# Kernel optimization log

Measured on AMD Instinct MI355X. Metric: run time of the kernel, lower is better.

Reference implementation:

```python
import jax, jax.numpy as jnp
import numpy as np


def setup_inputs() -> dict:
    key = jax.random.key(0)
    kq, kk, kv = jax.random.split(key, 3)
    # transpose_batch_sequence=True layout: [seq, batch, heads, head_dim]
    query = jax.random.normal(kq, (2048, 2, 32, 128), dtype=jnp.float32)
    k = jax.random.normal(kk, (2048, 2, 8, 128), dtype=jnp.float32)
    v = jax.random.normal(kv, (2048, 2, 8, 128), dtype=jnp.float32)
    return {"query": query, "key": k, "value": v}


def reference(query, key, value):
    # scale_attn_logits=True
    head_dim = query.shape[-1]
    q = query / jnp.sqrt(jnp.asarray(head_dim, dtype=query.dtype))
    h_q, h_kv = q.shape[-2], key.shape[-2]
    group_size = h_q // h_kv
    # [q, b, h_kv, g, d]
    gq = q.reshape((*q.shape[:2], h_kv, group_size, q.shape[-1]))
    # scores: [b, h_kv, g, q, k]
    attn = jnp.einsum('qbhgd,kbhd->bhgqk', gq, key)
    attn = jax.nn.softmax(attn, axis=-1)
    # output: [q, b, h_kv, g, d] -> [q, b, h_q, d]
    out = jnp.einsum('bhgqk,kbhd->qbhgd', attn, value)
    return out.reshape(query.shape)
```

## Files before the change

kernel.cpp:

```cpp
#include <hip/hip_runtime.h>

#define SEQ   2048
#define NB    2
#define NHQ   32
#define NHKV  8
#define HD    128
#define QTILE 128
#define QW    32
#define KVB   32
#define NT    (SEQ / KVB)
#define SCALE 0.08838834764831845f
#define QSCALE (0.08838834764831845f * 1.4426950408889634f)
#define THRL2 11.5f

#define QSTRIDE (NB * NHQ * HD)
#define KSTRIDE (NB * NHKV * HD)

typedef float f32x4  __attribute__((ext_vector_type(4)));
typedef float f32x16 __attribute__((ext_vector_type(16)));
typedef __bf16 bf16x8 __attribute__((ext_vector_type(8)));
typedef unsigned short ushort8 __attribute__((ext_vector_type(8)));
typedef unsigned int u32;
typedef unsigned int u32x2 __attribute__((ext_vector_type(2)));
typedef unsigned int u32x4 __attribute__((ext_vector_type(4)));

__device__ __forceinline__ unsigned short f2bf(float f) {
    union { float f; unsigned u; } c; c.f = f;
    return (unsigned short)((c.u + 0x7fffu + ((c.u >> 16) & 1u)) >> 16);
}

__device__ __forceinline__ void gload_lds16(const unsigned short* g, unsigned short* l) {
    __builtin_amdgcn_global_load_lds((const __attribute__((address_space(1))) u32*)g,
                                     (__attribute__((address_space(3))) u32*)l, 16, 0, 0);
}

__device__ __forceinline__ float ex2(float x) {
#if __has_builtin(__builtin_amdgcn_exp2f)
    return __builtin_amdgcn_exp2f(x);
#else
    return exp2f(x);
#endif
}

__device__ __forceinline__ u32 cvtpk(float lo, float hi) {
    u32 r;
    asm("v_cvt_pk_bf16_f32 %0, %1, %2" : "=v"(r) : "v"(lo), "v"(hi));
    return r;
}

__device__ __forceinline__ void pl32swap(u32& a, u32& b) {
#if __has_builtin(__builtin_amdgcn_permlane32_swap)
    u32x2 r = __builtin_amdgcn_permlane32_swap(a, b, false, false);
    a = r.x; b = r.y;
#else
    asm("v_permlane32_swap_b32 %0, %1" : "+v"(a), "+v"(b));
#endif
}

template <int B>
__device__ __forceinline__ bf16x8 make_pa(const f32x16 p) {
    u32 w0 = cvtpk(p[B + 0], p[B + 1]);
    u32 w2 = cvtpk(p[B + 4], p[B + 5]);
    pl32swap(w0, w2);
    u32 w1 = cvtpk(p[B + 2], p[B + 3]);
    u32 w3 = cvtpk(p[B + 6], p[B + 7]);
    pl32swap(w1, w3);
    u32x4 v = {w0, w1, w2, w3};
    return __builtin_bit_cast(bf16x8, v);
}

__global__ __launch_bounds__(256) void conv_k(const float* __restrict__ K,
                                              unsigned short* __restrict__ Kf) {
    __shared__ float tile[32][129];
    int t  = blockIdx.x & 63;
    int bh = blockIdx.x >> 6;
#pragma unroll
    for (int i = 0; i < 4; ++i) {
        int f4 = i * 256 + threadIdx.x;
        int r = f4 >> 5, d4 = (f4 & 31) * 4;
        float4 v = *(const float4*)(K + ((size_t)(t * 32 + r) * 16 + bh) * 128 + d4);
        tile[r][d4] = v.x; tile[r][d4 + 1] = v.y;
        tile[r][d4 + 2] = v.z; tile[r][d4 + 3] = v.w;
    }
    __syncthreads();
#pragma unroll
    for (int i = 0; i < 2; ++i) {
        int lin = i * 256 + threadIdx.x;
        int r = lin & 31, c = lin >> 5;
        ushort8 u;
#pragma unroll
        for (int j = 0; j < 8; ++j) u[j] = f2bf(tile[r][c * 8 + j]);
        *(ushort8*)&Kf[((size_t)(bh * 64 + t) * 16 + c) * 256 + r * 8] = u;
    }
}

__global__ __launch_bounds__(256) void conv_v(const float* __restrict__ V,
                                              unsigned short* __restrict__ Vf) {
    __shared__ float tile[32][129];
    int t  = blockIdx.x & 63;
    int bh = blockIdx.x >> 6;
#pragma unroll
    for (int i = 0; i < 4; ++i) {
        int f4 = i * 256 + threadIdx.x;
        int kv = f4 >> 5, d4 = (f4 & 31) * 4;
        float4 v = *(const float4*)(V + ((size_t)(t * 32 + kv) * 16 + bh) * 128 + d4);
        tile[kv][d4] = v.x; tile[kv][d4 + 1] = v.y;
        tile[kv][d4 + 2] = v.z; tile[kv][d4 + 3] = v.w;
    }
    __syncthreads();
#pragma unroll
    for (int i = 0; i < 2; ++i) {
        int lin = i * 256 + threadIdx.x;
        int r = lin & 31, db = (lin >> 5) & 3, cv = lin >> 7;
        ushort8 u;
#pragma unroll
        for (int j = 0; j < 8; ++j) u[j] = f2bf(tile[cv * 8 + j][db * 32 + r]);
        *(ushort8*)&Vf[((size_t)(bh * 64 + t) * 16 + cv * 4 + db) * 256 + r * 8] = u;
    }
}

__global__ __launch_bounds__(256, 3)
void attn_fwd10(const float* __restrict__ Q, const unsigned short* __restrict__ Kf,
                const unsigned short* __restrict__ Vf, float* __restrict__ O) {
    __shared__ __align__(16) unsigned char smemc[49152];

    const int tid  = threadIdx.x;
    const int w    = tid >> 6;
    const int lane = tid & 63;
    const int q31  = lane & 31;
    const int h    = lane >> 5;

    const int bid   = blockIdx.x;
    const int hkv   = bid & 7;
    const int rest  = bid >> 3;
    const int g     = rest & 3;
    const int b     = (rest >> 2) & 1;
    const int qtile = rest >> 3;
    const int hq    = hkv * 4 + g;

    const int qrow = qtile * QTILE + w * QW + q31;

    bf16x8 qf[8];
    {
        const float* qp = Q + (size_t)qrow * QSTRIDE + b * (NHQ * HD) + hq * HD;
#pragma unroll
        for (int s = 0; s < 8; ++s) {
            const float* p = qp + (2 * s + h) * 8;
            float4 f0 = *(const float4*)(p);
            float4 f1 = *(const float4*)(p + 4);
            ushort8 u;
            u[0] = f2bf(f0.x * QSCALE); u[1] = f2bf(f0.y * QSCALE);
            u[2] = f2bf(f0.z * QSCALE); u[3] = f2bf(f0.w * QSCALE);
            u[4] = f2bf(f1.x * QSCALE); u[5] = f2bf(f1.y * QSCALE);
            u[6] = f2bf(f1.z * QSCALE); u[7] = f2bf(f1.w * QSCALE);
            qf[s] = __builtin_bit_cast(bf16x8, u);
        }
    }

    const u32 kbase = h * 512 + q31 * 16;
    const u32 vbase = 24576 + h * 2048 + q31 * 16;

    f32x16 acc[4];
#pragma unroll
    for (int db = 0; db < 4; ++db) acc[db] = (f32x16)0.f;
    float mr = -3e38f, lsum = 0.f;

    const unsigned short* kbh = Kf + (size_t)(b * 8 + hkv) * 2048 * 128;
    const unsigned short* vbh = Vf + (size_t)(b * 8 + hkv) * 2048 * 128;

#define STAGE(sofb, tt) do {                                                           \
        _Pragma("unroll")                                                              \
        for (int i_ = 0; i_ < 2; ++i_) {                                               \
            const int c_ = w * 2 + i_;                                                 \
            gload_lds16(kbh + (size_t)(tt) * 4096 + c_ * 512 + lane * 8,               \
                        (unsigned short*)(smemc + (sofb) + c_ * 1024));                \
            gload_lds16(vbh + (size_t)(tt) * 4096 + c_ * 512 + lane * 8,               \
                        (unsigned short*)(smemc + 24576 + (sofb) + c_ * 1024));        \
        }                                                                              \
    } while (0)

    STAGE(0, 0);
    STAGE(8192, 1);
    int kof = 0;
    int sof = 16384;

    for (int t = 0; t < NT; ++t) {
        if (t < NT - 1) {
            asm volatile("s_waitcnt vmcnt(4)" ::: "memory");
        } else {
            asm volatile("s_waitcnt vmcnt(0)" ::: "memory");
        }
        __builtin_amdgcn_s_barrier();
        if (t + 2 < NT) STAGE(sof, t + 2);

        f32x16 sa = (f32x16)0.f;
        __builtin_amdgcn_s_setprio(1);
#pragma unroll
        for (int s = 0; s < 8; ++s) {
            bf16x8 kf = *(const bf16x8*)&smemc[kbase + s * 1024 + kof];
            sa = __builtin_amdgcn_mfma_f32_32x32x16_bf16(kf, qf[s], sa, 0, 0, 0);
        }
        __builtin_amdgcn_s_setprio(0);

        {
            float t0 = fmaxf(fmaxf(sa[0], sa[1]),   fmaxf(sa[2], sa[3]));
            float t1 = fmaxf(fmaxf(sa[4], sa[5]),   fmaxf(sa[6], sa[7]));
            float t2 = fmaxf(fmaxf(sa[8], sa[9]),   fmaxf(sa[10], sa[11]));
            float t3 = fmaxf(fmaxf(sa[12], sa[13]), fmaxf(sa[14], sa[15]));
            float tm = fmaxf(fmaxf(t0, t1), fmaxf(t2, t3));
            tm = fmaxf(tm, __shfl_xor(tm, 32));
            if (!__all(tm <= mr + THRL2)) {
                float mn   = fmaxf(mr, tm);
                float corr = ex2(mr - mn);
                lsum *= corr;
#pragma unroll
                for (int db = 0; db < 4; ++db)
#pragma unroll
                    for (int r = 0; r < 16; ++r) acc[db][r] *= corr;
                mr = mn;
            }
#pragma unroll
            for (int r = 0; r < 16; ++r) sa[r] = ex2(sa[r] - mr);
            float s0 = (sa[0] + sa[1]) + (sa[2] + sa[3]);
            float s1 = (sa[4] + sa[5]) + (sa[6] + sa[7]);
            float s2 = (sa[8] + sa[9]) + (sa[10] + sa[11]);
            float s3 = (sa[12] + sa[13]) + (sa[14] + sa[15]);
            lsum += (s0 + s1) + (s2 + s3);
        }

        bf16x8 pa[2];
        pa[0] = make_pa<0>(sa);
        pa[1] = make_pa<8>(sa);

        __builtin_amdgcn_s_setprio(1);
#pragma unroll
        for (int db = 0; db < 4; ++db) {
#pragma unroll
            for (int ks = 0; ks < 2; ++ks) {
                bf16x8 vf = *(const bf16x8*)&smemc[vbase + ks * 4096 + db * 512 + kof];
                acc[db] = __builtin_amdgcn_mfma_f32_32x32x16_bf16(vf, pa[ks], acc[db], 0, 0, 0);
            }
        }
        __builtin_amdgcn_s_setprio(0);

        kof = (kof == 16384) ? 0 : kof + 8192;
        sof = (sof == 16384) ? 0 : sof + 8192;
    }
#undef STAGE

    __syncthreads();
    lsum += __shfl_xor(lsum, 32);
    float invl = 1.f / lsum;
    float* ep = (float*)(void*)smemc + w * 2176;
    const int qtb = qtile * QTILE + w * QW;
    float* ob = O + b * (NHQ * HD) + hq * HD;

#pragma unroll
    for (int pass = 0; pass < 2; ++pass) {
#pragma unroll
        for (int db2 = 0; db2 < 2; ++db2) {
            const int db = pass * 2 + db2;
#pragma unroll
            for (int r = 0; r < 16; ++r)
                ep[q31 * 68 + db2 * 32 + (r & 3) + 8 * (r >> 2) + 4 * h] = acc[db][r] * invl;
        }
        __syncthreads();
#pragma unroll
        for (int i = 0; i < 8; ++i) {
            const int row = i * 4 + (lane >> 4);
            const int f4  = lane & 15;
            float4 val = *(const float4*)&ep[row * 68 + f4 * 4];
            *(float4*)(ob + (size_t)(qtb + row) * QSTRIDE + pass * 64 + f4 * 4) = val;
        }
        __syncthreads();
    }
}

#define KPAD  136
#define VPAD  72
#define PPAD  72
__global__ __launch_bounds__(512, 2)
void attn_fwd(const float* __restrict__ Q, const float* __restrict__ K,
              const float* __restrict__ V, float* __restrict__ O) {
    __shared__ __align__(16) unsigned short kbuf[64 * KPAD];
    __shared__ __align__(16) unsigned short vbuf[HD * VPAD];
    __shared__ __align__(16) unsigned short pbuf[8][16 * PPAD];

    const int tid = threadIdx.x;
    const int w = tid >> 6, lane = tid & 63;
    const int row16 = lane & 15, kg = lane >> 4;
    const int bid = blockIdx.x;
    const int qtile = bid & 7, g = (bid >> 3) & 3, b = (bid >> 5) & 1, hkv = bid >> 6;
    const int hq = hkv * 4 + g;
    const int qbase = qtile * 256 + w * 32;

    ushort8 qf[2][4];
#pragma unroll
    for (int s = 0; s < 2; ++s) {
        const int qrow = qbase + s * 16 + row16;
        const float* qp = Q + (size_t)qrow * QSTRIDE + b * (NHQ * HD) + hq * HD;
#pragma unroll
        for (int kk = 0; kk < 4; ++kk) {
            const float* p = qp + kk * 32 + kg * 8;
            float4 f0 = *(const float4*)(p);
            float4 f1 = *(const float4*)(p + 4);
            ushort8 u;
            u[0] = f2bf(f0.x * SCALE); u[1] = f2bf(f0.y * SCALE);
            u[2] = f2bf(f0.z * SCALE); u[3] = f2bf(f0.w * SCALE);
            u[4] = f2bf(f1.x * SCALE); u[5] = f2bf(f1.y * SCALE);
            u[6] = f2bf(f1.z * SCALE); u[7] = f2bf(f1.w * SCALE);
            qf[s][kk] = u;
        }
    }
    float m[2][4], lsum[2][4];
    f32x4 acco[2][8];
#pragma unroll
    for (int s = 0; s < 2; ++s)
#pragma unroll
        for (int r = 0; r < 4; ++r) { m[s][r] = -1e30f; lsum[s][r] = 0.f; }
#pragma unroll
    for (int s = 0; s < 2; ++s)
#pragma unroll
        for (int n = 0; n < 8; ++n) acco[s][n] = (f32x4)0.f;

    const float* kb0 = K + b * (NHKV * HD) + hkv * HD;
    const float* vb0 = V + b * (NHKV * HD) + hkv * HD;

    for (int kvt = 0; kvt < SEQ / 64; ++kvt) {
        const int kv0 = kvt * 64;
        __syncthreads();
        const float* kb = kb0 + (size_t)kv0 * KSTRIDE;
#pragma unroll
        for (int i = 0; i < 2; ++i) {
            int c = i * 512 + tid;
            int row = c >> 4, c8 = c & 15;
            const float* src = kb + (size_t)row * KSTRIDE + c8 * 8;
            float4 f0 = *(const float4*)(src);
            float4 f1 = *(const float4*)(src + 4);
            ushort8 u;
            u[0] = f2bf(f0.x); u[1] = f2bf(f0.y); u[2] = f2bf(f0.z); u[3] = f2bf(f0.w);
            u[4] = f2bf(f1.x); u[5] = f2bf(f1.y); u[6] = f2bf(f1.z); u[7] = f2bf(f1.w);
            *(ushort8*)&kbuf[row * KPAD + c8 * 8] = u;
        }
        const float* vb = vb0 + (size_t)kv0 * KSTRIDE;
#pragma unroll
        for (int i = 0; i < 4; ++i) {
            int f4i = i * 512 + tid;
            int kv = f4i >> 5, d0 = (f4i & 31) * 4;
            float4 v4 = *(const float4*)(vb + (size_t)kv * KSTRIDE + d0);
            vbuf[(d0 + 0) * VPAD + kv] = f2bf(v4.x);
            vbuf[(d0 + 1) * VPAD + kv] = f2bf(v4.y);
            vbuf[(d0 + 2) * VPAD + kv] = f2bf(v4.z);
            vbuf[(d0 + 3) * VPAD + kv] = f2bf(v4.w);
        }
        __syncthreads();

        f32x4 sa[2][4];
#pragma unroll
        for (int s = 0; s < 2; ++s)
#pragma unroll
            for (int n = 0; n < 4; ++n) sa[s][n] = (f32x4)0.f;
#pragma unroll
        for (int kk = 0; kk < 4; ++kk) {
#pragma unroll
            for (int n = 0; n < 4; ++n) {
                bf16x8 bfr = *(const bf16x8*)&kbuf[(n * 16 + row16) * KPAD + kk * 32 + kg * 8];
                sa[0][n] = __builtin_amdgcn_mfma_f32_16x16x32_bf16(
                    __builtin_bit_cast(bf16x8, qf[0][kk]), bfr, sa[0][n], 0, 0, 0);
                sa[1][n] = __builtin_amdgcn_mfma_f32_16x16x32_bf16(
                    __builtin_bit_cast(bf16x8, qf[1][kk]), bfr, sa[1][n], 0, 0, 0);
            }
        }
#pragma unroll
        for (int s = 0; s < 2; ++s) {
#pragma unroll
            for (int r = 0; r < 4; ++r) {
                float tm = fmaxf(fmaxf(sa[s][0][r], sa[s][1][r]), fmaxf(sa[s][2][r], sa[s][3][r]));
                tm = fmaxf(tm, __shfl_xor(tm, 1, 16));
                tm = fmaxf(tm, __shfl_xor(tm, 2, 16));
                tm = fmaxf(tm, __shfl_xor(tm, 4, 16));
                tm = fmaxf(tm, __shfl_xor(tm, 8, 16));
                float mn = fmaxf(m[s][r], tm);
                float corr = __expf(m[s][r] - mn);
                float ps = 0.f;
                int prow = kg * 4 + r;
#pragma unroll
                for (int n = 0; n < 4; ++n) {
                    float p = __expf(sa[s][n][r] - mn);
                    ps += p;
                    pbuf[w][prow * PPAD + n * 16 + row16] = f2bf(p);
                }
                ps += __shfl_xor(ps, 1, 16);
                ps += __shfl_xor(ps, 2, 16);
                ps += __shfl_xor(ps, 4, 16);
                ps += __shfl_xor(ps, 8, 16);
                lsum[s][r] = lsum[s][r] * corr + ps;
                m[s][r] = mn;
#pragma unroll
                for (int n8 = 0; n8 < 8; ++n8) acco[s][n8][r] *= corr;
            }
#pragma unroll
            for (int kk2 = 0; kk2 < 2; ++kk2) {
                bf16x8 pa = *(const bf16x8*)&pbuf[w][row16 * PPAD + kk2 * 32 + kg * 8];
#pragma unroll
                for (int n8 = 0; n8 < 8; ++n8) {
                    bf16x8 vf = *(const bf16x8*)&vbuf[(n8 * 16 + row16) * VPAD + kk2 * 32 + kg * 8];
                    acco[s][n8] = __builtin_amdgcn_mfma_f32_16x16x32_bf16(pa, vf, acco[s][n8], 0, 0, 0);
                }
            }
        }
    }
    float* ob = O + b * (NHQ * HD) + hq * HD;
#pragma unroll
    for (int s = 0; s < 2; ++s)
#pragma unroll
        for (int r = 0; r < 4; ++r) {
            float inv = 1.f / lsum[s][r];
            int qrow = qbase + s * 16 + kg * 4 + r;
            float* op = ob + (size_t)qrow * QSTRIDE;
#pragma unroll
            for (int n8 = 0; n8 < 8; ++n8)
                op[n8 * 16 + row16] = acco[s][n8][r] * inv;
        }
}

extern "C" void kernel_launch(void* const* d_in, const int* in_sizes, int n_in,
                              void* d_out, int out_size, void* d_ws, size_t ws_size,
                              hipStream_t stream) {
    (void)in_sizes; (void)n_in; (void)out_size;
    const float* Q = (const float*)d_in[0];
    const float* K = (const float*)d_in[1];
    const float* V = (const float*)d_in[2];
    float* Out = (float*)d_out;

    const size_t kv_elems = (size_t)16 * 2048 * 128;
    const size_t need = kv_elems * 2 * sizeof(unsigned short);

    if (ws_size >= need) {
        unsigned short* Kf = (unsigned short*)d_ws;
        unsigned short* Vf = Kf + kv_elems;
        conv_k<<<dim3(1024), dim3(256), 0, stream>>>(K, Kf);
        conv_v<<<dim3(1024), dim3(256), 0, stream>>>(V, Vf);
        attn_fwd10<<<dim3(1024), dim3(256), 0, stream>>>(Q, Kf, Vf, Out);
    } else {
        attn_fwd<<<dim3(512), dim3(512), 0, stream>>>(Q, K, V, Out);
    }
}
```

Before: 174.7 us.

## Switch to double-buffered K/V LDS to fit four blocks per CU

```diff
diff --git a/kernel.cpp b/kernel.cpp
--- a/kernel.cpp
+++ b/kernel.cpp
@@ -16,7 +16,9 @@
 #define QSTRIDE (NB * NHQ * HD)
 #define KSTRIDE (NB * NHKV * HD)
 
+typedef float f32x2  __attribute__((ext_vector_type(2)));
 typedef float f32x4  __attribute__((ext_vector_type(4)));
+typedef float f32x8  __attribute__((ext_vector_type(8)));
 typedef float f32x16 __attribute__((ext_vector_type(16)));
 typedef __bf16 bf16x8 __attribute__((ext_vector_type(8)));
 typedef unsigned short ushort8 __attribute__((ext_vector_type(8)));
@@ -69,6 +71,34 @@
     return __builtin_bit_cast(bf16x8, v);
 }
 
+__device__ __forceinline__ f32x8 lo8(f32x16 v) {
+    return __builtin_shufflevector(v, v, 0, 1, 2, 3, 4, 5, 6, 7);
+}
+__device__ __forceinline__ f32x8 hi8(f32x16 v) {
+    return __builtin_shufflevector(v, v, 8, 9, 10, 11, 12, 13, 14, 15);
+}
+__device__ __forceinline__ f32x4 lo4(f32x8 v) { return __builtin_shufflevector(v, v, 0, 1, 2, 3); }
+__device__ __forceinline__ f32x4 hi4(f32x8 v) { return __builtin_shufflevector(v, v, 4, 5, 6, 7); }
+
+__device__ __forceinline__ float vmax16(f32x16 v) {
+#if __has_builtin(__builtin_elementwise_max)
+    f32x8 a = __builtin_elementwise_max(lo8(v), hi8(v));
+    f32x4 b = __builtin_elementwise_max(lo4(a), hi4(a));
+    float c0 = fmaxf(b[0], b[2]), c1 = fmaxf(b[1], b[3]);
+    return fmaxf(c0, c1);
+#else
+    float m = v[0];
+#pragma unroll
+    for (int r = 1; r < 16; ++r) m = fmaxf(m, v[r]);
+    return m;
+#endif
+}
+__device__ __forceinline__ float vsum16(f32x16 v) {
+    f32x8 a = lo8(v) + hi8(v);
+    f32x4 b = lo4(a) + hi4(a);
+    return (b[0] + b[2]) + (b[1] + b[3]);
+}
+
 __global__ __launch_bounds__(256) void conv_k(const float* __restrict__ K,
                                               unsigned short* __restrict__ Kf) {
     __shared__ float tile[32][129];
@@ -119,10 +149,10 @@
     }
 }
 
-__global__ __launch_bounds__(256, 3)
-void attn_fwd10(const float* __restrict__ Q, const unsigned short* __restrict__ Kf,
+__global__ __launch_bounds__(256, 4)
+void attn_fwd11(const float* __restrict__ Q, const unsigned short* __restrict__ Kf,
                 const unsigned short* __restrict__ Vf, float* __restrict__ O) {
-    __shared__ __align__(16) unsigned char smemc[49152];
+    __shared__ __align__(16) unsigned char smemc[34816];
 
     const int tid  = threadIdx.x;
     const int w    = tid >> 6;
@@ -158,7 +188,7 @@
     }
 
     const u32 kbase = h * 512 + q31 * 16;
-    const u32 vbase = 24576 + h * 2048 + q31 * 16;
+    const u32 vbase = 8192 + h * 2048 + q31 * 16;
 
     f32x16 acc[4];
 #pragma unroll
@@ -175,23 +205,17 @@
             gload_lds16(kbh + (size_t)(tt) * 4096 + c_ * 512 + lane * 8,               \
                         (unsigned short*)(smemc + (sofb) + c_ * 1024));                \
             gload_lds16(vbh + (size_t)(tt) * 4096 + c_ * 512 + lane * 8,               \
-                        (unsigned short*)(smemc + 24576 + (sofb) + c_ * 1024));        \
+                        (unsigned short*)(smemc + (sofb) + 8192 + c_ * 1024));         \
         }                                                                              \
     } while (0)
 
     STAGE(0, 0);
-    STAGE(8192, 1);
     int kof = 0;
-    int sof = 16384;
 
     for (int t = 0; t < NT; ++t) {
-        if (t < NT - 1) {
-            asm volatile("s_waitcnt vmcnt(4)" ::: "memory");
-        } else {
-            asm volatile("s_waitcnt vmcnt(0)" ::: "memory");
-        }
+        asm volatile("s_waitcnt vmcnt(0)" ::: "memory");
         __builtin_amdgcn_s_barrier();
-        if (t + 2 < NT) STAGE(sof, t + 2);
+        if (t + 1 < NT) STAGE(kof ^ 16384, t + 1);
 
         f32x16 sa = (f32x16)0.f;
         __builtin_amdgcn_s_setprio(1);
@@ -203,29 +227,20 @@
         __builtin_amdgcn_s_setprio(0);
 
         {
-            float t0 = fmaxf(fmaxf(sa[0], sa[1]),   fmaxf(sa[2], sa[3]));
-            float t1 = fmaxf(fmaxf(sa[4], sa[5]),   fmaxf(sa[6], sa[7]));
-            float t2 = fmaxf(fmaxf(sa[8], sa[9]),   fmaxf(sa[10], sa[11]));
-            float t3 = fmaxf(fmaxf(sa[12], sa[13]), fmaxf(sa[14], sa[15]));
-            float tm = fmaxf(fmaxf(t0, t1), fmaxf(t2, t3));
+            float tm = vmax16(sa);
             tm = fmaxf(tm, __shfl_xor(tm, 32));
             if (!__all(tm <= mr + THRL2)) {
                 float mn   = fmaxf(mr, tm);
                 float corr = ex2(mr - mn);
                 lsum *= corr;
 #pragma unroll
-                for (int db = 0; db < 4; ++db)
-#pragma unroll
-                    for (int r = 0; r < 16; ++r) acc[db][r] *= corr;
+                for (int db = 0; db < 4; ++db) acc[db] = acc[db] * corr;
                 mr = mn;
             }
-#pragma unroll
-            for (int r = 0; r < 16; ++r) sa[r] = ex2(sa[r] - mr);
-            float s0 = (sa[0] + sa[1]) + (sa[2] + sa[3]);
-            float s1 = (sa[4] + sa[5]) + (sa[6] + sa[7]);
-            float s2 = (sa[8] + sa[9]) + (sa[10] + sa[11]);
-            float s3 = (sa[12] + sa[13]) + (sa[14] + sa[15]);
-            lsum += (s0 + s1) + (s2 + s3);
+            sa = sa - mr;
+#pragma unroll
+            for (int r = 0; r < 16; ++r) sa[r] = ex2(sa[r]);
+            lsum += vsum16(sa);
         }
 
         bf16x8 pa[2];
@@ -243,8 +258,7 @@
         }
         __builtin_amdgcn_s_setprio(0);
 
-        kof = (kof == 16384) ? 0 : kof + 8192;
-        sof = (sof == 16384) ? 0 : sof + 8192;
+        kof ^= 16384;
     }
 #undef STAGE
 
@@ -441,7 +455,7 @@
         unsigned short* Vf = Kf + kv_elems;
         conv_k<<<dim3(1024), dim3(256), 0, stream>>>(K, Kf);
         conv_v<<<dim3(1024), dim3(256), 0, stream>>>(V, Vf);
-        attn_fwd10<<<dim3(1024), dim3(256), 0, stream>>>(Q, Kf, Vf, Out);
+        attn_fwd11<<<dim3(1024), dim3(256), 0, stream>>>(Q, Kf, Vf, Out);
     } else {
         attn_fwd<<<dim3(512), dim3(512), 0, stream>>>(Q, K, V, Out);
     }
```

Measured after the change: 186.2 us. 1.07x slower.
